# Optimization experiments

Hardware: AMD Instinct MI355X
Metric: run time of the kernel (lower is better)

## Reference

```python
import jax, jax.numpy as jnp
import numpy as np

N = 20000
T = 6890
FEAT = 128
DEG = 32
K = 6


def setup_inputs() -> dict:
    key = jax.random.key(0)
    k1, k2, k3, k4, k5 = jax.random.split(key, 5)
    source_feats = jax.random.normal(k1, (N, FEAT), dtype=jnp.float32)
    target_feats = jax.random.normal(k2, (T, FEAT), dtype=jnp.float32)
    target_points = jax.random.normal(k3, (T, 3), dtype=jnp.float32)
    pos = jax.random.normal(k4, (N, 3), dtype=jnp.float32)
    # kNN-style graph: every center node (row) has exactly DEG neighbors (col)
    row = jnp.repeat(jnp.arange(N, dtype=jnp.int32), DEG)
    col = jax.random.randint(k5, (N * DEG,), 0, N, dtype=jnp.int32)
    edge_index = jnp.stack([row, col], axis=0)  # [2, E]
    return {"source_feats": source_feats, "target_feats": target_feats,
            "target_points": target_points, "pos": pos, "edge_index": edge_index}


def reference(source_feats, target_feats, target_points, pos, edge_index):
    n = source_feats.shape[0]
    # --- soft retrieval against template ---
    dp = source_feats @ target_feats.T                                 # [N,T]
    dists = ((source_feats * source_feats).sum(-1, keepdims=True)
             - 2.0 * dp
             + (target_feats * target_feats).sum(-1)[None, :])         # [N,T]
    neg_scores, indices = jax.lax.top_k(-dists, K)                      # [N,K]
    scores = jax.nn.softmax(neg_scores, axis=-1)                        # [N,K]
    selected = target_points[indices]                                   # [N,K,3]
    predicted = (selected * scores[..., None]).sum(-2)                  # [N,3]

    row, col = edge_index[0], edge_index[1]
    src_nb = pos[col]                                                   # [E,3]
    tgt_nb = predicted[col]                                             # [E,3]

    cnt = jax.ops.segment_sum(jnp.ones(row.shape, src_nb.dtype), row,
                              num_segments=n)
    cnt = jnp.maximum(cnt, 1.0)[:, None]                                # [N,1]
    src_centers = jax.ops.segment_sum(src_nb, row, num_segments=n) / cnt
    tgt_centers = jax.ops.segment_sum(tgt_nb, row, num_segments=n) / cnt

    sd = src_nb - src_centers[row]                                      # [E,3]
    td = tgt_nb - tgt_centers[row]                                      # [E,3]
    edge_mat = sd[:, :, None] * td[:, None, :]                          # [E,3,3] outer products
    pm = jax.ops.segment_sum(edge_mat, row, num_segments=n)             # [N,3,3]

    # --- Procrustes via batched 3x3 SVD (torch.svd: A = U S V^T; jnp: A = U S Vh => V^T = Vh) ---
    U, S, Vh = jnp.linalg.svd(pm)
    R0 = jax.lax.stop_gradient(U @ Vh)
    detR0 = jnp.linalg.det(R0)
    d = jax.lax.stop_gradient(
        jnp.stack([jnp.ones_like(detR0), jnp.ones_like(detR0), detR0], -1))  # [N,3]
    R = (U * d[:, None, :]) @ Vh                                        # U @ diag(d) @ V^T
    trans = tgt_centers - jnp.einsum('nij,nj->ni', R, src_centers)      # [N,3]

    # --- residual under neighbor transforms ---
    transformed = jnp.einsum('eij,ej->ei', R[col], src_nb) + trans[col]  # [E,3]
    res = transformed - tgt_nb
    dsts = (res * res).sum(-1, keepdims=True)                           # [E,1]
    dst = jax.ops.segment_sum(dsts, row, num_segments=n) / cnt          # [N,1]
    return R, trans, dst
```

## Files before the change

kernel.cpp:

```cpp
#include <hip/hip_runtime.h>
#include <math.h>

#define NS 20000
#define TT 6890
#define TPAD 6912
#define FE 128
#define EDG 640000
#define DEG 32

#define RPB 80
#define NCB 4
#define CBW 1728
#define NH 5

typedef __attribute__((ext_vector_type(8))) short short8;
typedef __attribute__((ext_vector_type(4))) float floatx4;
typedef unsigned int uint;

__device__ __forceinline__ unsigned short f2bf(float f) {
  unsigned int u = __float_as_uint(f);
  return (unsigned short)((u + 0x7fffu + ((u >> 16) & 1u)) >> 16);
}

__device__ __forceinline__ uint med3u(uint a, uint b, uint c) {
  uint d;
  asm("v_med3_u32 %0, %1, %2, %3" : "=v"(d) : "v"(a), "v"(b), "v"(c));
  return d;
}
__device__ __forceinline__ void ins6(uint* a, uint t) {
  a[5] = med3u(a[4], a[5], t);
  a[4] = med3u(a[3], a[4], t);
  a[3] = med3u(a[2], a[3], t);
  a[2] = med3u(a[1], a[2], t);
  a[1] = med3u(a[0], a[1], t);
  a[0] = min(a[0], t);
}
__device__ __forceinline__ void ins12(uint* a, uint t) {
  a[11] = med3u(a[10], a[11], t);
  a[10] = med3u(a[9], a[10], t);
  a[9]  = med3u(a[8], a[9], t);
  a[8]  = med3u(a[7], a[8], t);
  a[7]  = med3u(a[6], a[7], t);
  a[6]  = med3u(a[5], a[6], t);
  a[5]  = med3u(a[4], a[5], t);
  a[4]  = med3u(a[3], a[4], t);
  a[3]  = med3u(a[2], a[3], t);
  a[2]  = med3u(a[1], a[2], t);
  a[1]  = med3u(a[0], a[1], t);
  a[0]  = min(a[0], t);
}

__global__ void tn_cast_kernel(const float* __restrict__ tf, float* __restrict__ tn,
                               float* __restrict__ tn256,
                               unsigned short* __restrict__ tfbx) {
  int gid = blockIdx.x * blockDim.x + threadIdx.x;
  int w = gid >> 6;
  int lane = gid & 63;
  if (w >= TPAD) return;
  unsigned short* base = tfbx + (size_t)w * 128;
  int jj = lane >> 2;
  int soff = ((jj ^ (w & 7)) << 3) + (lane & 3) * 2;
  if (w < TT) {
    const float* p = tf + (size_t)w * FE;
    float a = p[lane];
    float b = p[lane + 64];
    float s = a * a + b * b;
#pragma unroll
    for (int off = 32; off > 0; off >>= 1) s += __shfl_xor(s, off);
    if (lane == 0) { tn[w] = s; tn256[w] = -0.5f * (s + 256.0f); }
    ushort2 o;
    o.x = f2bf(p[2 * lane]);
    o.y = f2bf(p[2 * lane + 1]);
    *reinterpret_cast<ushort2*>(base + soff) = o;
  } else {
    if (lane == 0) { tn[w] = 1e30f; tn256[w] = -1.5e38f; }
    ushort2 z; z.x = 0; z.y = 0;
    *reinterpret_cast<ushort2*>(base + soff) = z;
  }
}

union SmemK1 {
  unsigned short Bs[RPB * 128];
  uint pk[RPB][24];
};

__device__ __forceinline__ void mfma4_sel(
    short8 a0, short8 a1, short8 a2, short8 a3,
    short8 b0, short8 b1, short8 b2, short8 b3,
    float4 t4, uint ck, uint* kqh) {
  floatx4 acc = (floatx4){t4.x, t4.y, t4.z, t4.w};
  acc = __builtin_amdgcn_mfma_f32_16x16x32_bf16(a0, b0, acc, 0, 0, 0);
  acc = __builtin_amdgcn_mfma_f32_16x16x32_bf16(a1, b1, acc, 0, 0, 0);
  acc = __builtin_amdgcn_mfma_f32_16x16x32_bf16(a2, b2, acc, 0, 0, 0);
  acc = __builtin_amdgcn_mfma_f32_16x16x32_bf16(a3, b3, acc, 0, 0, 0);
#pragma unroll
  for (int r = 0; r < 4; ++r) {
    uint t = (__float_as_uint(acc[r]) & 0xFFFFE000u) | (ck + (uint)r);
    ins6(kqh, t);
  }
}

__global__ __launch_bounds__(256, 2) void topk_kernel(
    const float* __restrict__ sf, const unsigned short* __restrict__ tfbx,
    const float* __restrict__ tn256, uint* __restrict__ pkall) {
  __shared__ SmemK1 u;
  const int tid = threadIdx.x;
  const int lane = tid & 63;
  const int wv = tid >> 6;
  const int q = lane >> 4;
  const int m = lane & 15;
  const int rb = (int)blockIdx.x >> 2;
  const int cb = (int)blockIdx.x & 3;
  const int row0 = rb * RPB;
  const int cbase = cb * CBW;

#pragma unroll
  for (int t = 0; t < 5; ++t) {
    int c = tid + t * 256;
    int rr = c >> 4, jj = c & 15;
    const float* src = sf + (size_t)(row0 + rr) * FE + jj * 8;
    float4 f0 = *reinterpret_cast<const float4*>(src);
    float4 f1 = *reinterpret_cast<const float4*>(src + 4);
    union { unsigned short us[8]; uint4 v; } tt;
    tt.us[0] = f2bf(f0.x); tt.us[1] = f2bf(f0.y);
    tt.us[2] = f2bf(f0.z); tt.us[3] = f2bf(f0.w);
    tt.us[4] = f2bf(f1.x); tt.us[5] = f2bf(f1.y);
    tt.us[6] = f2bf(f1.z); tt.us[7] = f2bf(f1.w);
    *reinterpret_cast<uint4*>(u.Bs + rr * 128 + ((jj ^ (rr & 7)) << 3)) = tt.v;
  }

  uint kq[NH][6];
#pragma unroll
  for (int h = 0; h < NH; ++h)
#pragma unroll
    for (int k = 0; k < 6; ++k) kq[h][k] = 0xFFFFFFFFu;

  int rdB[4];
  int aoff[4];
  const int ax = m & 7;
#pragma unroll
  for (int ks = 0; ks < 4; ++ks) {
    int slot = (ks * 4 + q) ^ ax;
    rdB[ks] = m * 128 + (slot << 3);
    aoff[ks] = slot << 3;
  }
  const unsigned short* abase = tfbx + (size_t)(cbase + wv * 16 + m) * 128;
  const uint ck0 = (uint)(cbase + wv * 16 + q * 4);

  __syncthreads();

  short8 bf[NH][4];
#pragma unroll
  for (int h = 0; h < NH; ++h) {
    const unsigned short* bb = u.Bs + h * 2048;
#pragma unroll
    for (int ks = 0; ks < 4; ++ks)
      bf[h][ks] = *reinterpret_cast<const short8*>(bb + rdB[ks]);
  }

  for (int s = 0; s < 27; ++s) {
    const unsigned short* ap = abase + (size_t)s * 8192;
    short8 a0 = *reinterpret_cast<const short8*>(ap + aoff[0]);
    short8 a1 = *reinterpret_cast<const short8*>(ap + aoff[1]);
    short8 a2 = *reinterpret_cast<const short8*>(ap + aoff[2]);
    short8 a3 = *reinterpret_cast<const short8*>(ap + aoff[3]);
    const float* tb = tn256 + cbase + s * 64 + wv * 16 + q * 4;
    float4 t4 = *reinterpret_cast<const float4*>(tb);
    const uint ck = ck0 + (uint)(s * 64);
#pragma unroll
    for (int h = 0; h < NH; ++h)
      mfma4_sel(a0, a1, a2, a3, bf[h][0], bf[h][1], bf[h][2], bf[h][3],
                t4, ck, kq[h]);
  }

#pragma unroll
  for (int h = 0; h < NH; ++h) {
#pragma unroll
    for (int st = 16; st <= 32; st <<= 1) {
      uint inc[6];
#pragma unroll
      for (int k = 0; k < 6; ++k) inc[k] = __shfl_xor(kq[h][k], st);
#pragma unroll
      for (int k = 0; k < 6; ++k) ins6(kq[h], inc[k]);
    }
  }
  __syncthreads();
  if (q == 0) {
#pragma unroll
    for (int h = 0; h < NH; ++h)
#pragma unroll
      for (int k = 0; k < 6; ++k) u.pk[h * 16 + m][wv * 6 + k] = kq[h][k];
  }
  __syncthreads();

  if (tid < RPB) {
    uint md[12];
#pragma unroll
    for (int k = 0; k < 12; ++k) md[k] = 0xFFFFFFFFu;
    for (int j = 0; j < 24; ++j) ins12(md, u.pk[tid][j]);
    uint* dst = pkall + (size_t)(row0 + tid) * 48 + cb * 12;
#pragma unroll
    for (int k = 0; k < 12; ++k) dst[k] = md[k];
  }
}

__global__ __launch_bounds__(256) void merge_kernel(
    const float* __restrict__ sf, const float* __restrict__ tf,
    const float* __restrict__ tn, const uint* __restrict__ pkall,
    const float* __restrict__ tp, float* __restrict__ pred) {
  __shared__ float sv[4][24];
  __shared__ int   sc[4][24];
  const int lane = threadIdx.x & 63;
  const int wv = threadIdx.x >> 6;
  const int row = (int)blockIdx.x * 4 + wv;
  uint k0 = 0xFFFFFFFFu;
  if (lane < 48) k0 = pkall[(size_t)row * 48 + lane];
  int r0 = 0;
  for (int j = 0; j < 48; ++j) {
    uint a = __shfl(k0, j);
    r0 += (a < k0) ? 1 : 0;
  }
  if (lane < 48 && r0 < 24) {
    int col = (int)(k0 & 0x1FFFu);
    const float* srow = sf + (size_t)row * FE;
    const float* trow = tf + (size_t)col * FE;
    float accv = 0.f;
#pragma unroll 8
    for (int kk = 0; kk < FE; kk += 4) {
      float4 av = *reinterpret_cast<const float4*>(srow + kk);
      float4 bv = *reinterpret_cast<const float4*>(trow + kk);
      accv += av.x * bv.x + av.y * bv.y + av.z * bv.z + av.w * bv.w;
    }
    sv[wv][r0] = tn[col] - 2.f * accv;
    sc[wv][r0] = col;
  }
  __syncthreads();
  if (lane == 0) {
    float sd[6]; int sp6[6];
#pragma unroll
    for (int k = 0; k < 6; ++k) { sd[k] = 1e30f; sp6[k] = 0; }
    for (int j = 0; j < 24; ++j) {
      float v = sv[wv][j];
      if (v < sd[5]) {
        sd[5] = v; sp6[5] = j;
#pragma unroll
        for (int k = 4; k >= 0; --k) {
          if (sd[k + 1] < sd[k]) {
            float tvv = sd[k]; sd[k] = sd[k + 1]; sd[k + 1] = tvv;
            int tii = sp6[k]; sp6[k] = sp6[k + 1]; sp6[k + 1] = tii;
          }
        }
      }
    }
    float wgt[6]; float wsum = 0.f;
#pragma unroll
    for (int k = 0; k < 6; ++k) { wgt[k] = __expf(sd[0] - sd[k]); wsum += wgt[k]; }
    float inv = 1.f / wsum;
    float px = 0.f, py = 0.f, pz = 0.f;
#pragma unroll
    for (int k = 0; k < 6; ++k) {
      float scv = wgt[k] * inv;
      const float* qq = tp + (size_t)sc[wv][sp6[k]] * 3;
      px += scv * qq[0]; py += scv * qq[1]; pz += scv * qq[2];
    }
    pred[row * 3 + 0] = px;
    pred[row * 3 + 1] = py;
    pred[row * 3 + 2] = pz;
  }
}

__global__ __launch_bounds__(64) void proc_kernel(
    const int* __restrict__ colp, const float* __restrict__ pos,
    const float* __restrict__ pred, float* __restrict__ Rout,
    float* __restrict__ tout, float* __restrict__ qnorm) {
  int i = blockIdx.x * blockDim.x + threadIdx.x;
  if (i >= NS) return;
  int4 cia[8];
#pragma unroll
  for (int t = 0; t < 8; ++t)
    cia[t] = reinterpret_cast<const int4*>(colp + (size_t)i * DEG)[t];
  const int* cidx = reinterpret_cast<const int*>(cia);

  double sp[3] = {0, 0, 0}, sq[3] = {0, 0, 0};
  double spq[3][3] = {{0, 0, 0}, {0, 0, 0}, {0, 0, 0}};
#pragma unroll
  for (int e = 0; e < DEG; ++e) {
    int c = cidx[e];
    double p0 = pos[c * 3], p1 = pos[c * 3 + 1], p2 = pos[c * 3 + 2];
    double q0 = pred[c * 3], q1 = pred[c * 3 + 1], q2 = pred[c * 3 + 2];
    sp[0] += p0; sp[1] += p1; sp[2] += p2;
    sq[0] += q0; sq[1] += q1; sq[2] += q2;
    spq[0][0] += p0 * q0; spq[0][1] += p0 * q1; spq[0][2] += p0 * q2;
    spq[1][0] += p1 * q0; spq[1][1] += p1 * q1; spq[1][2] += p1 * q2;
    spq[2][0] += p2 * q0; spq[2][1] += p2 * q1; spq[2][2] += p2 * q2;
  }
  const double inv = 1.0 / 32.0;
  double A[3][3], sc[3], tcn[3];
  for (int a = 0; a < 3; ++a) {
    sc[a] = sp[a] * inv;
    tcn[a] = sq[a] * inv;
  }
  for (int a = 0; a < 3; ++a)
    for (int b = 0; b < 3; ++b) A[a][b] = spq[a][b] - sp[a] * sq[b] * inv;

  double S[3][3];
  for (int a = 0; a < 3; ++a)
    for (int b = 0; b < 3; ++b)
      S[a][b] = A[0][a] * A[0][b] + A[1][a] * A[1][b] + A[2][a] * A[2][b];
  double V[3][3] = {{1, 0, 0}, {0, 1, 0}, {0, 0, 1}};
  const int JP[3] = {0, 0, 1}, JQ[3] = {1, 2, 2};
  for (int sweep = 0; sweep < 6; ++sweep) {
    for (int r = 0; r < 3; ++r) {
      int p = JP[r], q = JQ[r];
      double apq = S[p][q];
      if (fabs(apq) < 1e-300) continue;
      double theta = (S[q][q] - S[p][p]) / (2.0 * apq);
      double t = copysign(1.0 / (fabs(theta) + sqrt(theta * theta + 1.0)), theta);
      double c = 1.0 / sqrt(t * t + 1.0);
      double s = t * c;
      double spp = S[p][p], sqq = S[q][q];
      S[p][p] = spp - t * apq;
      S[q][q] = sqq + t * apq;
      S[p][q] = 0.0; S[q][p] = 0.0;
      int k = 3 - p - q;
      double skp = S[k][p], skq = S[k][q];
      S[k][p] = S[p][k] = c * skp - s * skq;
      S[k][q] = S[q][k] = s * skp + c * skq;
      for (int mth = 0; mth < 3; ++mth) {
        double vp = V[mth][p], vq = V[mth][q];
        V[mth][p] = c * vp - s * vq;
        V[mth][q] = s * vp + c * vq;
      }
    }
  }
  double lam[3] = {S[0][0], S[1][1], S[2][2]};
  int i0 = 0, i1 = 1, i2 = 2, tmp;
  if (lam[i0] < lam[i1]) { tmp = i0; i0 = i1; i1 = tmp; }
  if (lam[i0] < lam[i2]) { tmp = i0; i0 = i2; i2 = tmp; }
  if (lam[i1] < lam[i2]) { tmp = i1; i1 = i2; i2 = tmp; }
  double v0[3] = {V[0][i0], V[1][i0], V[2][i0]};
  double v1[3] = {V[0][i1], V[1][i1], V[2][i1]};
  double v2[3] = {V[0][i2], V[1][i2], V[2][i2]};

  double Av0[3], Av1[3], Av2[3];
  for (int a = 0; a < 3; ++a) {
    Av0[a] = A[a][0] * v0[0] + A[a][1] * v0[1] + A[a][2] * v0[2];
    Av1[a] = A[a][0] * v1[0] + A[a][1] * v1[1] + A[a][2] * v1[2];
    Av2[a] = A[a][0] * v2[0] + A[a][1] * v2[1] + A[a][2] * v2[2];
  }
  double n0 = fmax(sqrt(Av0[0]*Av0[0] + Av0[1]*Av0[1] + Av0[2]*Av0[2]), 1e-300);
  double u0[3] = {Av0[0] / n0, Av0[1] / n0, Av0[2] / n0};
  double proj = u0[0]*Av1[0] + u0[1]*Av1[1] + u0[2]*Av1[2];
  double u1[3] = {Av1[0] - proj * u0[0], Av1[1] - proj * u0[1], Av1[2] - proj * u0[2]};
  double n1 = fmax(sqrt(u1[0]*u1[0] + u1[1]*u1[1] + u1[2]*u1[2]), 1e-300);
  u1[0] /= n1; u1[1] /= n1; u1[2] /= n1;
  double w[3] = {u0[1]*u1[2] - u0[2]*u1[1],
                 u0[2]*u1[0] - u0[0]*u1[2],
                 u0[0]*u1[1] - u0[1]*u1[0]};
  double dotw = Av2[0]*w[0] + Av2[1]*w[1] + Av2[2]*w[2];
  double sgn = (dotw < 0.0) ? -1.0 : 1.0;
  double detA = A[0][0]*(A[1][1]*A[2][2] - A[1][2]*A[2][1])
              - A[0][1]*(A[1][0]*A[2][2] - A[1][2]*A[2][0])
              + A[0][2]*(A[1][0]*A[2][1] - A[1][1]*A[2][0]);
  double d3 = ((detA < 0.0) ? -1.0 : 1.0) * sgn;

  double R[3][3];
  for (int a = 0; a < 3; ++a)
    for (int b = 0; b < 3; ++b)
      R[a][b] = u0[a]*v0[b] + u1[a]*v1[b] + d3 * w[a]*v2[b];

  for (int a = 0; a < 3; ++a)
    for (int b = 0; b < 3; ++b) Rout[i * 9 + a * 3 + b] = (float)R[a][b];
  double tr_[3];
  for (int a = 0; a < 3; ++a) {
    tr_[a] = tcn[a] - (R[a][0]*sc[0] + R[a][1]*sc[1] + R[a][2]*sc[2]);
    tout[i * 3 + a] = (float)tr_[a];
  }
  double pxi = pos[i * 3], pyi = pos[i * 3 + 1], pzi = pos[i * 3 + 2];
  double r0 = R[0][0]*pxi + R[0][1]*pyi + R[0][2]*pzi + tr_[0] - pred[i * 3];
  double r1 = R[1][0]*pxi + R[1][1]*pyi + R[1][2]*pzi + tr_[1] - pred[i * 3 + 1];
  double r2 = R[2][0]*pxi + R[2][1]*pyi + R[2][2]*pzi + tr_[2] - pred[i * 3 + 2];
  qnorm[i] = (float)(r0 * r0 + r1 * r1 + r2 * r2);
}

__global__ __launch_bounds__(64) void dst_kernel(
    const int* __restrict__ colp, const float* __restrict__ qn,
    float* __restrict__ dout) {
  int i = blockIdx.x * blockDim.x + threadIdx.x;
  if (i >= NS) return;
  int4 cia[8];
#pragma unroll
  for (int t = 0; t < 8; ++t)
    cia[t] = reinterpret_cast<const int4*>(colp + (size_t)i * DEG)[t];
  const int* cidx = reinterpret_cast<const int*>(cia);
  float s = 0.f;
#pragma unroll
  for (int e = 0; e < DEG; ++e) s += qn[cidx[e]];
  dout[i] = s * (1.0f / 32.0f);
}

extern "C" void kernel_launch(void* const* d_in, const int* in_sizes, int n_in,
                              void* d_out, int out_size, void* d_ws, size_t ws_size,
                              hipStream_t stream) {
  const float* sf  = (const float*)d_in[0];
  const float* tf  = (const float*)d_in[1];
  const float* tp  = (const float*)d_in[2];
  const float* pos = (const float*)d_in[3];
  const int*   ei  = (const int*)d_in[4];
  float* out = (float*)d_out;
  char* ws = (char*)d_ws;
  float*          tn    = (float*)(ws);
  float*          tn256 = (float*)(ws + 28672);
  float*          pred  = (float*)(ws + 57344);
  uint*           pkall = (uint*)(ws + 297344);
  unsigned short* tfbx  = (unsigned short*)(ws + 4137344);
  float*          qn    = (float*)(ws + 4137344);
  const int* colp = ei + EDG;

  tn_cast_kernel<<<(TPAD * 64) / 256, 256, 0, stream>>>(tf, tn, tn256, tfbx);
  topk_kernel<<<(NS / RPB) * NCB, 256, 0, stream>>>(sf, tfbx, tn256, pkall);
  merge_kernel<<<NS / 4, 256, 0, stream>>>(sf, tf, tn, pkall, tp, pred);
  proc_kernel<<<(NS + 63) / 64, 64, 0, stream>>>(colp, pos, pred, out,
                                                 out + NS * 9, qn);
  dst_kernel<<<(NS + 63) / 64, 64, 0, stream>>>(colp, qn, out + NS * 12);
}
```

Measured before the change: 227.6 us.

## Prefetch A tiles in topk, cooperative rescoring in merge, split proc edges

```diff
diff --git a/kernel.cpp b/kernel.cpp
--- a/kernel.cpp
+++ b/kernel.cpp
@@ -158,19 +158,27 @@
       bf[h][ks] = *reinterpret_cast<const short8*>(bb + rdB[ks]);
   }
 
+  short8 a0 = *reinterpret_cast<const short8*>(abase + aoff[0]);
+  short8 a1 = *reinterpret_cast<const short8*>(abase + aoff[1]);
+  short8 a2 = *reinterpret_cast<const short8*>(abase + aoff[2]);
+  short8 a3 = *reinterpret_cast<const short8*>(abase + aoff[3]);
+  float4 t4 = *reinterpret_cast<const float4*>(tn256 + cbase + wv * 16 + q * 4);
+
   for (int s = 0; s < 27; ++s) {
-    const unsigned short* ap = abase + (size_t)s * 8192;
-    short8 a0 = *reinterpret_cast<const short8*>(ap + aoff[0]);
-    short8 a1 = *reinterpret_cast<const short8*>(ap + aoff[1]);
-    short8 a2 = *reinterpret_cast<const short8*>(ap + aoff[2]);
-    short8 a3 = *reinterpret_cast<const short8*>(ap + aoff[3]);
-    const float* tb = tn256 + cbase + s * 64 + wv * 16 + q * 4;
-    float4 t4 = *reinterpret_cast<const float4*>(tb);
+    const int sn = (s < 26) ? s + 1 : 26;
+    const unsigned short* apn = abase + (size_t)sn * 8192;
+    short8 na0 = *reinterpret_cast<const short8*>(apn + aoff[0]);
+    short8 na1 = *reinterpret_cast<const short8*>(apn + aoff[1]);
+    short8 na2 = *reinterpret_cast<const short8*>(apn + aoff[2]);
+    short8 na3 = *reinterpret_cast<const short8*>(apn + aoff[3]);
+    float4 nt4 = *reinterpret_cast<const float4*>(
+        tn256 + cbase + sn * 64 + wv * 16 + q * 4);
     const uint ck = ck0 + (uint)(s * 64);
 #pragma unroll
     for (int h = 0; h < NH; ++h)
       mfma4_sel(a0, a1, a2, a3, bf[h][0], bf[h][1], bf[h][2], bf[h][3],
                 t4, ck, kq[h]);
+    a0 = na0; a1 = na1; a2 = na2; a3 = na3; t4 = nt4;
   }
 
 #pragma unroll
@@ -220,19 +228,33 @@
     uint a = __shfl(k0, j);
     r0 += (a < k0) ? 1 : 0;
   }
-  if (lane < 48 && r0 < 24) {
-    int col = (int)(k0 & 0x1FFFu);
-    const float* srow = sf + (size_t)row * FE;
+  const int g = lane >> 2;
+  const int c4 = lane & 3;
+  float4 sfc[8];
+  const float* srow = sf + (size_t)row * FE;
+#pragma unroll
+  for (int it = 0; it < 8; ++it)
+    sfc[it] = *reinterpret_cast<const float4*>(srow + (it * 4 + c4) * 4);
+#pragma unroll
+  for (int p = 0; p < 3; ++p) {
+    const int j = p * 16 + g;
+    const uint kj = __shfl(k0, j);
+    const int rj = __shfl(r0, j);
+    const int col = (int)(kj & 0x1FFFu);
     const float* trow = tf + (size_t)col * FE;
-    float accv = 0.f;
-#pragma unroll 8
-    for (int kk = 0; kk < FE; kk += 4) {
-      float4 av = *reinterpret_cast<const float4*>(srow + kk);
-      float4 bv = *reinterpret_cast<const float4*>(trow + kk);
-      accv += av.x * bv.x + av.y * bv.y + av.z * bv.z + av.w * bv.w;
-    }
-    sv[wv][r0] = tn[col] - 2.f * accv;
-    sc[wv][r0] = col;
+    float acc = 0.f;
+#pragma unroll
+    for (int it = 0; it < 8; ++it) {
+      float4 bv = *reinterpret_cast<const float4*>(trow + (it * 4 + c4) * 4);
+      float4 av = sfc[it];
+      acc += av.x * bv.x + av.y * bv.y + av.z * bv.z + av.w * bv.w;
+    }
+    acc += __shfl_xor(acc, 1);
+    acc += __shfl_xor(acc, 2);
+    if (c4 == 0 && rj < 24) {
+      sv[wv][rj] = tn[col] - 2.f * acc;
+      sc[wv][rj] = col;
+    }
   }
   __syncthreads();
   if (lane == 0) {
@@ -269,22 +291,24 @@
   }
 }
 
-__global__ __launch_bounds__(64) void proc_kernel(
+__global__ __launch_bounds__(256) void proc_kernel(
     const int* __restrict__ colp, const float* __restrict__ pos,
     const float* __restrict__ pred, float* __restrict__ Rout,
     float* __restrict__ tout, float* __restrict__ qnorm) {
-  int i = blockIdx.x * blockDim.x + threadIdx.x;
+  int t = blockIdx.x * blockDim.x + threadIdx.x;
+  int i = t >> 2;
+  int l = t & 3;
   if (i >= NS) return;
-  int4 cia[8];
-#pragma unroll
-  for (int t = 0; t < 8; ++t)
-    cia[t] = reinterpret_cast<const int4*>(colp + (size_t)i * DEG)[t];
+  int4 cia[2];
+#pragma unroll
+  for (int tt = 0; tt < 2; ++tt)
+    cia[tt] = reinterpret_cast<const int4*>(colp + (size_t)i * DEG + l * 8)[tt];
   const int* cidx = reinterpret_cast<const int*>(cia);
 
   double sp[3] = {0, 0, 0}, sq[3] = {0, 0, 0};
   double spq[3][3] = {{0, 0, 0}, {0, 0, 0}, {0, 0, 0}};
 #pragma unroll
-  for (int e = 0; e < DEG; ++e) {
+  for (int e = 0; e < 8; ++e) {
     int c = cidx[e];
     double p0 = pos[c * 3], p1 = pos[c * 3 + 1], p2 = pos[c * 3 + 2];
     double q0 = pred[c * 3], q1 = pred[c * 3 + 1], q2 = pred[c * 3 + 2];
@@ -294,6 +318,17 @@
     spq[1][0] += p1 * q0; spq[1][1] += p1 * q1; spq[1][2] += p1 * q2;
     spq[2][0] += p2 * q0; spq[2][1] += p2 * q1; spq[2][2] += p2 * q2;
   }
+#pragma unroll
+  for (int mask = 1; mask <= 2; mask <<= 1) {
+#pragma unroll
+    for (int a = 0; a < 3; ++a) {
+      sp[a] += __shfl_xor(sp[a], mask);
+      sq[a] += __shfl_xor(sq[a], mask);
+#pragma unroll
+      for (int b = 0; b < 3; ++b) spq[a][b] += __shfl_xor(spq[a][b], mask);
+    }
+  }
+
   const double inv = 1.0 / 32.0;
   double A[3][3], sc[3], tcn[3];
   for (int a = 0; a < 3; ++a) {
@@ -315,12 +350,12 @@
       double apq = S[p][q];
       if (fabs(apq) < 1e-300) continue;
       double theta = (S[q][q] - S[p][p]) / (2.0 * apq);
-      double t = copysign(1.0 / (fabs(theta) + sqrt(theta * theta + 1.0)), theta);
-      double c = 1.0 / sqrt(t * t + 1.0);
-      double s = t * c;
+      double t2 = copysign(1.0 / (fabs(theta) + sqrt(theta * theta + 1.0)), theta);
+      double c = 1.0 / sqrt(t2 * t2 + 1.0);
+      double s = t2 * c;
       double spp = S[p][p], sqq = S[q][q];
-      S[p][p] = spp - t * apq;
-      S[q][q] = sqq + t * apq;
+      S[p][p] = spp - t2 * apq;
+      S[q][q] = sqq + t2 * apq;
       S[p][q] = 0.0; S[q][p] = 0.0;
       int k = 3 - p - q;
       double skp = S[k][p], skq = S[k][q];
@@ -369,18 +404,20 @@
     for (int b = 0; b < 3; ++b)
       R[a][b] = u0[a]*v0[b] + u1[a]*v1[b] + d3 * w[a]*v2[b];
 
-  for (int a = 0; a < 3; ++a)
-    for (int b = 0; b < 3; ++b) Rout[i * 9 + a * 3 + b] = (float)R[a][b];
-  double tr_[3];
-  for (int a = 0; a < 3; ++a) {
-    tr_[a] = tcn[a] - (R[a][0]*sc[0] + R[a][1]*sc[1] + R[a][2]*sc[2]);
-    tout[i * 3 + a] = (float)tr_[a];
-  }
-  double pxi = pos[i * 3], pyi = pos[i * 3 + 1], pzi = pos[i * 3 + 2];
-  double r0 = R[0][0]*pxi + R[0][1]*pyi + R[0][2]*pzi + tr_[0] - pred[i * 3];
-  double r1 = R[1][0]*pxi + R[1][1]*pyi + R[1][2]*pzi + tr_[1] - pred[i * 3 + 1];
-  double r2 = R[2][0]*pxi + R[2][1]*pyi + R[2][2]*pzi + tr_[2] - pred[i * 3 + 2];
-  qnorm[i] = (float)(r0 * r0 + r1 * r1 + r2 * r2);
+  if (l == 0) {
+    for (int a = 0; a < 3; ++a)
+      for (int b = 0; b < 3; ++b) Rout[i * 9 + a * 3 + b] = (float)R[a][b];
+    double tr_[3];
+    for (int a = 0; a < 3; ++a) {
+      tr_[a] = tcn[a] - (R[a][0]*sc[0] + R[a][1]*sc[1] + R[a][2]*sc[2]);
+      tout[i * 3 + a] = (float)tr_[a];
+    }
+    double pxi = pos[i * 3], pyi = pos[i * 3 + 1], pzi = pos[i * 3 + 2];
+    double r0 = R[0][0]*pxi + R[0][1]*pyi + R[0][2]*pzi + tr_[0] - pred[i * 3];
+    double r1 = R[1][0]*pxi + R[1][1]*pyi + R[1][2]*pzi + tr_[1] - pred[i * 3 + 1];
+    double r2 = R[2][0]*pxi + R[2][1]*pyi + R[2][2]*pzi + tr_[2] - pred[i * 3 + 2];
+    qnorm[i] = (float)(r0 * r0 + r1 * r1 + r2 * r2);
+  }
 }
 
 __global__ __launch_bounds__(64) void dst_kernel(
@@ -420,7 +457,7 @@
   tn_cast_kernel<<<(TPAD * 64) / 256, 256, 0, stream>>>(tf, tn, tn256, tfbx);
   topk_kernel<<<(NS / RPB) * NCB, 256, 0, stream>>>(sf, tfbx, tn256, pkall);
   merge_kernel<<<NS / 4, 256, 0, stream>>>(sf, tf, tn, pkall, tp, pred);
-  proc_kernel<<<(NS + 63) / 64, 64, 0, stream>>>(colp, pos, pred, out,
-                                                 out + NS * 9, qn);
+  proc_kernel<<<(NS * 4 + 255) / 256, 256, 0, stream>>>(colp, pos, pred, out,
+                                                        out + NS * 9, qn);
   dst_kernel<<<(NS + 63) / 64, 64, 0, stream>>>(colp, qn, out + NS * 12);
 }
```

Result: faster. 207.5 us (-8.8%).
